# Optimization experiments

Hardware: AMD Instinct MI355X
Metric: run time of the kernel (lower is better)

The kernel has to match this reference:

```python
import jax, jax.numpy as jnp
import numpy as np

K = 3  # number of propagation hops in SGConv


def setup_inputs() -> dict:
    key = jax.random.key(0)
    k1, k2, k3, k4 = jax.random.split(key, 4)
    N, E, F_in, F_out = 100000, 1600000, 32, 64
    x = jax.random.normal(k1, (N, F_in), dtype=jnp.float32)
    edge_index = jax.random.randint(k2, (2, E), 0, N, dtype=jnp.int64)
    # Linear(in_channels, hidden_channels) params, torch layout: W [out, in], b [out]
    lim = 1.0 / np.sqrt(F_in)
    W = jax.random.uniform(k3, (F_out, F_in), minval=-lim, maxval=lim, dtype=jnp.float32)
    b = jax.random.uniform(k4, (F_out,), minval=-lim, maxval=lim, dtype=jnp.float32)
    return {"x": x, "edge_index": edge_index, "W": W, "b": b}


def reference(x, edge_index, W, b):
    N = x.shape[0]
    # gcn_norm: add self-loops with weight 1, symmetric normalization
    loop = jnp.arange(N, dtype=edge_index.dtype)
    src = jnp.concatenate([edge_index[0], loop])  # [E+N] message sources (x_j)
    dst = jnp.concatenate([edge_index[1], loop])  # [E+N] aggregation targets
    ones = jnp.ones(src.shape[0], dtype=x.dtype)
    deg = jax.ops.segment_sum(ones, dst, num_segments=N)  # in-degree incl. self-loop
    dinv = jnp.where(deg > 0, jax.lax.rsqrt(deg), 0.0)
    norm = dinv[src] * dinv[dst]  # [E+N]
    # K hops of normalized sparse propagation: x <- \hat{A} x
    h = x
    for _ in range(K):
        h = jax.ops.segment_sum(norm[:, None] * h[src], dst, num_segments=N)
    # final linear transform
    return h @ W.T + b
```

## Files before the change

### kernel.cpp

```cpp
#include <hip/hip_runtime.h>


#define F_IN 32
#define F_OUT 64
#define SB_SHIFT 13
#define MAXSB 16
#define SUB_SHIFT 9
#define SUB (1 << SUB_SHIFT)
#define EPB1 2048
#define EPB2 4096
#define SCAP 147456
#define SUBCAP 12288
#define BPS (SCAP / EPB2)

typedef float f4 __attribute__((ext_vector_type(4)));
typedef _Float16 h4 __attribute__((ext_vector_type(4)));
typedef int i2 __attribute__((ext_vector_type(2)));

__global__ __launch_bounds__(256) void k_bin1(const int* __restrict__ ei,
                                              int* __restrict__ scur,
                                              unsigned* __restrict__ b1, int E) {
    __shared__ unsigned stage[EPB1];
    __shared__ unsigned char bid[EPB1];
    __shared__ int hist[MAXSB], lscan[MAXSB], lbase[MAXSB], fcur[MAXSB];
    int tid = threadIdx.x;
    int base = blockIdx.x * EPB1;
    int cnt = E - base; if (cnt > EPB1) cnt = EPB1;

    if (tid < MAXSB) hist[tid] = 0;
    __syncthreads();
    for (int k = 0; k < EPB1 / 256; ++k) {
        int i = base + k * 256 + tid;
        if (i < E) atomicAdd(&hist[ei[E + i] >> SB_SHIFT], 1);
    }
    __syncthreads();
    if (tid < 64) {
        int c = (tid < MAXSB) ? hist[tid] : 0;
        int inc = c;
#pragma unroll
        for (int off = 1; off < MAXSB; off <<= 1) {
            int t = __shfl_up(inc, off);
            if (tid >= off) inc += t;
        }
        if (tid < MAXSB) {
            lscan[tid] = inc - c;
            fcur[tid] = inc - c;
            lbase[tid] = c ? atomicAdd(&scur[tid], c) : 0;
        }
    }
    __syncthreads();
    for (int k = 0; k < EPB1 / 256; ++k) {
        int i = base + k * 256 + tid;
        if (i < E) {
            unsigned s = (unsigned)ei[i];
            unsigned d = (unsigned)ei[E + i];
            int b = d >> SB_SHIFT;
            int loc = atomicAdd(&fcur[b], 1);
            stage[loc] = (s << SB_SHIFT) | (d & ((1u << SB_SHIFT) - 1));
            bid[loc] = (unsigned char)b;
        }
    }
    __syncthreads();
    for (int k = 0; k < EPB1 / 256; ++k) {
        int idx = k * 256 + tid;
        if (idx < cnt) {
            int b = bid[idx];
            b1[(size_t)b * SCAP + lbase[b] + (idx - lscan[b])] = stage[idx];
        }
    }
}

__global__ __launch_bounds__(256) void k_bin2(const unsigned* __restrict__ b1,
                                              const int* __restrict__ scur,
                                              int* __restrict__ subcur,
                                              unsigned* __restrict__ b2) {
    int sb = blockIdx.x / BPS;
    int base = (blockIdx.x % BPS) * EPB2;
    int count = scur[sb];
    if (base >= count) return;
    int cnt = count - base; if (cnt > EPB2) cnt = EPB2;
    const unsigned* src = b1 + (size_t)sb * SCAP + base;

    __shared__ unsigned stage[EPB2];
    __shared__ unsigned char bid[EPB2];
    __shared__ int hist[16], lscan[16], lbase[16], fcur[16];
    int tid = threadIdx.x;
    if (tid < 16) hist[tid] = 0;
    __syncthreads();
    for (int k = 0; k < EPB2 / 256; ++k) {
        int i = k * 256 + tid;
        if (i < cnt) atomicAdd(&hist[(src[i] >> SUB_SHIFT) & 15], 1);
    }
    __syncthreads();
    if (tid < 64) {
        int c = (tid < 16) ? hist[tid] : 0;
        int inc = c;
#pragma unroll
        for (int off = 1; off < 16; off <<= 1) {
            int t = __shfl_up(inc, off);
            if (tid >= off) inc += t;
        }
        if (tid < 16) {
            lscan[tid] = inc - c;
            fcur[tid] = inc - c;
            lbase[tid] = c ? atomicAdd(&subcur[sb * 16 + tid], c) : 0;
        }
    }
    __syncthreads();
    for (int k = 0; k < EPB2 / 256; ++k) {
        int i = k * 256 + tid;
        if (i < cnt) {
            unsigned r = src[i];
            int b = (r >> SUB_SHIFT) & 15;
            int loc = atomicAdd(&fcur[b], 1);
            stage[loc] = ((r >> SB_SHIFT) << SUB_SHIFT) | (r & (SUB - 1));
            bid[loc] = (unsigned char)b;
        }
    }
    __syncthreads();
    for (int k = 0; k < EPB2 / 256; ++k) {
        int idx = k * 256 + tid;
        if (idx < cnt) {
            int b = bid[idx];
            b2[(size_t)(sb * 16 + b) * SUBCAP + lbase[b] + (idx - lscan[b])] = stage[idx];
        }
    }
}

__global__ __launch_bounds__(512) void k_fill3(const unsigned* __restrict__ b2,
                                               const int* __restrict__ subcur,
                                               float* __restrict__ dinv,
                                               i2* __restrict__ rp2,
                                               int* __restrict__ col, int N) {
    __shared__ unsigned stage[SUBCAP];
    __shared__ int h[SUB];
    __shared__ int wsum[8];
    int tid = threadIdx.x;
    int g = blockIdx.x;
    int count = subcur[g];
    int sbase = g * SUBCAP;

    h[tid] = 0;
    for (int e = tid; e < count; e += 512) stage[e] = b2[(size_t)sbase + e];
    __syncthreads();
    for (int e = tid; e < count; e += 512) atomicAdd(&h[stage[e] & (SUB - 1)], 1);
    __syncthreads();

    int deg = h[tid];
    int lane = tid & 63, wid = tid >> 6;
    int inc = deg;
#pragma unroll
    for (int off = 1; off < 64; off <<= 1) {
        int t = __shfl_up(inc, off);
        if (lane >= off) inc += t;
    }
    if (lane == 63) wsum[wid] = inc;
    __syncthreads();
    if (wid == 0) {
        int v = (lane < 8) ? wsum[lane] : 0;
#pragma unroll
        for (int off = 1; off < 8; off <<= 1) {
            int t = __shfl_up(v, off);
            if (lane >= off) v += t;
        }
        if (lane < 8) wsum[lane] = v;
    }
    __syncthreads();
    int incl = inc + (wid ? wsum[wid - 1] : 0);
    int excl = incl - deg;

    int node = (g << SUB_SHIFT) + tid;
    if (node < N) {
        dinv[node] = rsqrtf(1.0f + (float)deg);
        rp2[node] = (i2){sbase + excl, sbase + incl};
    }
    h[tid] = excl;
    __syncthreads();

    for (int e = tid; e < count; e += 512) {
        unsigned r = stage[e];
        int slot = sbase + atomicAdd(&h[r & (SUB - 1)], 1);
        col[slot] = (int)(r >> SUB_SHIFT);
    }
}

__global__ void k_prescale(const f4* __restrict__ x, const float* __restrict__ dinv,
                           h4* __restrict__ g, int N8) {
    int t = blockIdx.x * blockDim.x + threadIdx.x;
    if (t < N8) {
        f4 v = dinv[t >> 3] * x[t];
        g[t] = __builtin_convertvector(v, h4);
    }
}

__global__ __launch_bounds__(256) void k_hop_gather(const i2* __restrict__ rp2,
                                                    const int* __restrict__ col,
                                                    const float* __restrict__ dinv,
                                                    const h4* __restrict__ gin,
                                                    h4* __restrict__ gout,
                                                    int N, int final_hop) {
    int t = blockIdx.x * blockDim.x + threadIdx.x;
    int n = t >> 3;
    if (n >= N) return;
    int q = t & 7;
    i2 r2 = rp2[n];
    int e0 = r2.x, e1 = r2.y;
    f4 a0 = __builtin_convertvector(gin[n * 8 + q], f4);
    f4 a1 = {0.f, 0.f, 0.f, 0.f};
    int e = e0;
    for (; e + 3 < e1; e += 4) {
        int s0 = col[e], s1 = col[e + 1], s2 = col[e + 2], s3 = col[e + 3];
        h4 h0 = gin[s0 * 8 + q];
        h4 h1 = gin[s1 * 8 + q];
        h4 h2 = gin[s2 * 8 + q];
        h4 h3 = gin[s3 * 8 + q];
        a0 += __builtin_convertvector(h0, f4);
        a1 += __builtin_convertvector(h1, f4);
        a0 += __builtin_convertvector(h2, f4);
        a1 += __builtin_convertvector(h3, f4);
    }
    for (; e < e1; ++e) a0 += __builtin_convertvector(gin[col[e] * 8 + q], f4);
    float di = dinv[n];
    float sc = final_hop ? di : di * di;
    f4 r = sc * (a0 + a1);
    gout[n * 8 + q] = __builtin_convertvector(r, h4);
}

__global__ __launch_bounds__(256) void k_linear(const _Float16* __restrict__ h,
                                                const float* __restrict__ W,
                                                const float* __restrict__ b,
                                                float* __restrict__ out, int N) {
    __shared__ float Wl[F_OUT][F_IN + 1];
    __shared__ float hl[4][F_IN];
    int tid = threadIdx.x;
    for (int idx = tid; idx < F_OUT * F_IN; idx += 256) {
        Wl[idx >> 5][idx & 31] = W[idx];
    }
    int node0 = blockIdx.x * 4;
    if (tid < 4 * F_IN) {
        int n = tid >> 5, f = tid & 31;
        int node = node0 + n;
        hl[n][f] = (node < N) ? (float)h[node * F_IN + f] : 0.0f;
    }
    __syncthreads();
    int n = tid >> 6;
    int o = tid & 63;
    int node = node0 + n;
    if (node < N) {
        float acc = b[o];
#pragma unroll
        for (int f = 0; f < F_IN; ++f) acc += hl[n][f] * Wl[o][f];
        out[node * F_OUT + o] = acc;
    }
}

extern "C" void kernel_launch(void* const* d_in, const int* in_sizes, int n_in,
                              void* d_out, int out_size, void* d_ws, size_t ws_size,
                              hipStream_t stream) {
    const float* x  = (const float*)d_in[0];
    const int*   ei = (const int*)d_in[1];
    const float* W  = (const float*)d_in[2];
    const float* b  = (const float*)d_in[3];
    float* out = (float*)d_out;

    const int N = in_sizes[0] / F_IN;
    const int E = in_sizes[1] / 2;
    const int NSB  = (N + (1 << SB_SHIFT) - 1) >> SB_SHIFT;
    const int NSUB = (N + SUB - 1) >> SUB_SHIFT;

    int* scur   = (int*)d_ws;
    int* subcur = scur + MAXSB;
    i2*  rp2    = (i2*)(subcur + MAXSB * 16);
    float* dinv = (float*)(rp2 + N);
    unsigned* b1 = (unsigned*)(((uintptr_t)(dinv + N) + 255) & ~(uintptr_t)255);
    unsigned* b2 = b1 + (size_t)MAXSB * SCAP;
    int* col     = (int*)(b2 + (size_t)MAXSB * 16 * SUBCAP);
    _Float16* hA = (_Float16*)(((uintptr_t)(col + (size_t)MAXSB * 16 * SUBCAP) + 255)
                               & ~(uintptr_t)255);
    _Float16* hB  = hA + (size_t)N * F_IN;
    _Float16* hB2 = hB + (size_t)N * F_IN;

    const int B = 256;
    dim3 blk(B);

    hipMemsetAsync(scur, 0, (MAXSB + MAXSB * 16) * sizeof(int), stream);

    k_bin1<<<dim3((E + EPB1 - 1) / EPB1), blk, 0, stream>>>(ei, scur, b1, E);
    k_bin2<<<dim3(NSB * BPS), blk, 0, stream>>>(b1, scur, subcur, b2);

    k_fill3<<<dim3(NSUB), dim3(512), 0, stream>>>(b2, subcur, dinv, rp2, col, N);

    const int N8 = N * 8;
    k_prescale<<<dim3((N8 + B - 1) / B), blk, 0, stream>>>((const f4*)x, dinv, (h4*)hA, N8);

    dim3 gHop(((size_t)N * 8 + B - 1) / B);
    k_hop_gather<<<gHop, blk, 0, stream>>>(rp2, col, dinv, (const h4*)hA, (h4*)hB, N, 0);
    k_hop_gather<<<gHop, blk, 0, stream>>>(rp2, col, dinv, (const h4*)hB, (h4*)hB2, N, 0);
    k_hop_gather<<<gHop, blk, 0, stream>>>(rp2, col, dinv, (const h4*)hB2, (h4*)hA, N, 1);

    k_linear<<<dim3((N + 3) / 4), blk, 0, stream>>>(hA, W, b, out, N);
}
```

Baseline: 223.6 us.

## Fuse final hop with linear layer and cache edge records in registers during binning

The third propagation hop is merged with the final linear transform. Each block gathers 32 nodes into shared memory and computes 8 outputs per thread, which removes the fp16 round trip of the last hop and one kernel launch. The binning kernels now keep the records loaded in the histogram pass in registers instead of reading global memory a second time, and bin2 drops the shared bucket-id array by recomputing the bucket from the staged record. The fused kernel reloads W into shared memory for every 32 nodes and does more register work per thread.

Result: faster. 212.3 us (-5.1%).

```diff
diff --git a/kernel.cpp b/kernel.cpp
--- a/kernel.cpp
+++ b/kernel.cpp
@@ -21,17 +21,28 @@
                                               int* __restrict__ scur,
                                               unsigned* __restrict__ b1, int E) {
     __shared__ unsigned stage[EPB1];
-    __shared__ unsigned char bid[EPB1];
+    __shared__ unsigned char bidl[EPB1];
     __shared__ int hist[MAXSB], lscan[MAXSB], lbase[MAXSB], fcur[MAXSB];
+    unsigned rec[EPB1 / 256];
+    int      bk[EPB1 / 256];
     int tid = threadIdx.x;
     int base = blockIdx.x * EPB1;
     int cnt = E - base; if (cnt > EPB1) cnt = EPB1;
 
     if (tid < MAXSB) hist[tid] = 0;
     __syncthreads();
+#pragma unroll
     for (int k = 0; k < EPB1 / 256; ++k) {
         int i = base + k * 256 + tid;
-        if (i < E) atomicAdd(&hist[ei[E + i] >> SB_SHIFT], 1);
+        bk[k] = -1;
+        if (i < E) {
+            unsigned s = (unsigned)ei[i];
+            unsigned d = (unsigned)ei[E + i];
+            int b = d >> SB_SHIFT;
+            rec[k] = (s << SB_SHIFT) | (d & ((1u << SB_SHIFT) - 1));
+            bk[k] = b;
+            atomicAdd(&hist[b], 1);
+        }
     }
     __syncthreads();
     if (tid < 64) {
@@ -49,22 +60,19 @@
         }
     }
     __syncthreads();
+#pragma unroll
     for (int k = 0; k < EPB1 / 256; ++k) {
-        int i = base + k * 256 + tid;
-        if (i < E) {
-            unsigned s = (unsigned)ei[i];
-            unsigned d = (unsigned)ei[E + i];
-            int b = d >> SB_SHIFT;
-            int loc = atomicAdd(&fcur[b], 1);
-            stage[loc] = (s << SB_SHIFT) | (d & ((1u << SB_SHIFT) - 1));
-            bid[loc] = (unsigned char)b;
+        if (bk[k] >= 0) {
+            int loc = atomicAdd(&fcur[bk[k]], 1);
+            stage[loc] = rec[k];
+            bidl[loc] = (unsigned char)bk[k];
         }
     }
     __syncthreads();
     for (int k = 0; k < EPB1 / 256; ++k) {
         int idx = k * 256 + tid;
         if (idx < cnt) {
-            int b = bid[idx];
+            int b = bidl[idx];
             b1[(size_t)b * SCAP + lbase[b] + (idx - lscan[b])] = stage[idx];
         }
     }
@@ -82,14 +90,20 @@
     const unsigned* src = b1 + (size_t)sb * SCAP + base;
 
     __shared__ unsigned stage[EPB2];
-    __shared__ unsigned char bid[EPB2];
     __shared__ int hist[16], lscan[16], lbase[16], fcur[16];
+    unsigned rec[EPB2 / 256];
     int tid = threadIdx.x;
     if (tid < 16) hist[tid] = 0;
     __syncthreads();
+#pragma unroll
     for (int k = 0; k < EPB2 / 256; ++k) {
         int i = k * 256 + tid;
-        if (i < cnt) atomicAdd(&hist[(src[i] >> SUB_SHIFT) & 15], 1);
+        rec[k] = 0xFFFFFFFFu;
+        if (i < cnt) {
+            unsigned r = src[i];
+            rec[k] = r;
+            atomicAdd(&hist[(r >> SUB_SHIFT) & 15], 1);
+        }
     }
     __syncthreads();
     if (tid < 64) {
@@ -107,22 +121,22 @@
         }
     }
     __syncthreads();
+#pragma unroll
     for (int k = 0; k < EPB2 / 256; ++k) {
-        int i = k * 256 + tid;
-        if (i < cnt) {
-            unsigned r = src[i];
-            int b = (r >> SUB_SHIFT) & 15;
+        if (rec[k] != 0xFFFFFFFFu) {
+            int b = (rec[k] >> SUB_SHIFT) & 15;
             int loc = atomicAdd(&fcur[b], 1);
-            stage[loc] = ((r >> SB_SHIFT) << SUB_SHIFT) | (r & (SUB - 1));
-            bid[loc] = (unsigned char)b;
+            stage[loc] = rec[k];
         }
     }
     __syncthreads();
     for (int k = 0; k < EPB2 / 256; ++k) {
         int idx = k * 256 + tid;
         if (idx < cnt) {
-            int b = bid[idx];
-            b2[(size_t)(sb * 16 + b) * SUBCAP + lbase[b] + (idx - lscan[b])] = stage[idx];
+            unsigned r = stage[idx];
+            int b = (r >> SUB_SHIFT) & 15;
+            unsigned packed = ((r >> SB_SHIFT) << SUB_SHIFT) | (r & (SUB - 1));
+            b2[(size_t)(sb * 16 + b) * SUBCAP + lbase[b] + (idx - lscan[b])] = packed;
         }
     }
 }
@@ -197,8 +211,7 @@
                                                     const int* __restrict__ col,
                                                     const float* __restrict__ dinv,
                                                     const h4* __restrict__ gin,
-                                                    h4* __restrict__ gout,
-                                                    int N, int final_hop) {
+                                                    h4* __restrict__ gout, int N) {
     int t = blockIdx.x * blockDim.x + threadIdx.x;
     int n = t >> 3;
     if (n >= N) return;
@@ -221,36 +234,69 @@
     }
     for (; e < e1; ++e) a0 += __builtin_convertvector(gin[col[e] * 8 + q], f4);
     float di = dinv[n];
-    float sc = final_hop ? di : di * di;
+    float sc = di * di;
     f4 r = sc * (a0 + a1);
     gout[n * 8 + q] = __builtin_convertvector(r, h4);
 }
 
-__global__ __launch_bounds__(256) void k_linear(const _Float16* __restrict__ h,
-                                                const float* __restrict__ W,
-                                                const float* __restrict__ b,
-                                                float* __restrict__ out, int N) {
+__global__ __launch_bounds__(256) void k_hop3_linear(const i2* __restrict__ rp2,
+                                                     const int* __restrict__ col,
+                                                     const float* __restrict__ dinv,
+                                                     const h4* __restrict__ gin,
+                                                     const float* __restrict__ W,
+                                                     const float* __restrict__ bias,
+                                                     float* __restrict__ out, int N) {
     __shared__ float Wl[F_OUT][F_IN + 1];
-    __shared__ float hl[4][F_IN];
+    __shared__ float hl[32][F_IN + 1];
     int tid = threadIdx.x;
-    for (int idx = tid; idx < F_OUT * F_IN; idx += 256) {
+    for (int idx = tid; idx < F_OUT * F_IN; idx += 256)
         Wl[idx >> 5][idx & 31] = W[idx];
-    }
-    int node0 = blockIdx.x * 4;
-    if (tid < 4 * F_IN) {
-        int n = tid >> 5, f = tid & 31;
-        int node = node0 + n;
-        hl[n][f] = (node < N) ? (float)h[node * F_IN + f] : 0.0f;
-    }
-    __syncthreads();
-    int n = tid >> 6;
-    int o = tid & 63;
-    int node = node0 + n;
-    if (node < N) {
-        float acc = b[o];
-#pragma unroll
-        for (int f = 0; f < F_IN; ++f) acc += hl[n][f] * Wl[o][f];
-        out[node * F_OUT + o] = acc;
+
+    int nl = tid >> 3;
+    int q = tid & 7;
+    int n = blockIdx.x * 32 + nl;
+    if (n < N) {
+        i2 r2 = rp2[n];
+        int e0 = r2.x, e1 = r2.y;
+        f4 a0 = __builtin_convertvector(gin[n * 8 + q], f4);
+        f4 a1 = {0.f, 0.f, 0.f, 0.f};
+        int e = e0;
+        for (; e + 3 < e1; e += 4) {
+            int s0 = col[e], s1 = col[e + 1], s2 = col[e + 2], s3 = col[e + 3];
+            h4 h0 = gin[s0 * 8 + q];
+            h4 h1 = gin[s1 * 8 + q];
+            h4 h2 = gin[s2 * 8 + q];
+            h4 h3 = gin[s3 * 8 + q];
+            a0 += __builtin_convertvector(h0, f4);
+            a1 += __builtin_convertvector(h1, f4);
+            a0 += __builtin_convertvector(h2, f4);
+            a1 += __builtin_convertvector(h3, f4);
+        }
+        for (; e < e1; ++e) a0 += __builtin_convertvector(gin[col[e] * 8 + q], f4);
+        float di = dinv[n];
+        f4 r = di * (a0 + a1);
+        hl[nl][q * 4 + 0] = r.x;
+        hl[nl][q * 4 + 1] = r.y;
+        hl[nl][q * 4 + 2] = r.z;
+        hl[nl][q * 4 + 3] = r.w;
+    }
+    __syncthreads();
+    int obase = q * 8;
+    if (n < N) {
+        float acc[8];
+#pragma unroll
+        for (int j = 0; j < 8; ++j) acc[j] = bias[obase + j];
+#pragma unroll
+        for (int f = 0; f < F_IN; ++f) {
+            float hv = hl[nl][f];
+#pragma unroll
+            for (int j = 0; j < 8; ++j) acc[j] += hv * Wl[obase + j][f];
+        }
+        float* op = out + (size_t)n * F_OUT + obase;
+        f4 v0 = {acc[0], acc[1], acc[2], acc[3]};
+        f4 v1 = {acc[4], acc[5], acc[6], acc[7]};
+        *(f4*)op = v0;
+        *(f4*)(op + 4) = v1;
     }
 }
 
@@ -265,7 +311,6 @@
 
     const int N = in_sizes[0] / F_IN;
     const int E = in_sizes[1] / 2;
-    const int NSB  = (N + (1 << SB_SHIFT) - 1) >> SB_SHIFT;
     const int NSUB = (N + SUB - 1) >> SUB_SHIFT;
 
     int* scur   = (int*)d_ws;
@@ -286,7 +331,8 @@
     hipMemsetAsync(scur, 0, (MAXSB + MAXSB * 16) * sizeof(int), stream);
 
     k_bin1<<<dim3((E + EPB1 - 1) / EPB1), blk, 0, stream>>>(ei, scur, b1, E);
-    k_bin2<<<dim3(NSB * BPS), blk, 0, stream>>>(b1, scur, subcur, b2);
+    k_bin2<<<dim3(((N + (1 << SB_SHIFT) - 1) >> SB_SHIFT) * BPS), blk, 0, stream>>>(
+        b1, scur, subcur, b2);
 
     k_fill3<<<dim3(NSUB), dim3(512), 0, stream>>>(b2, subcur, dinv, rp2, col, N);
 
@@ -294,9 +340,9 @@
     k_prescale<<<dim3((N8 + B - 1) / B), blk, 0, stream>>>((const f4*)x, dinv, (h4*)hA, N8);
 
     dim3 gHop(((size_t)N * 8 + B - 1) / B);
-    k_hop_gather<<<gHop, blk, 0, stream>>>(rp2, col, dinv, (const h4*)hA, (h4*)hB, N, 0);
-    k_hop_gather<<<gHop, blk, 0, stream>>>(rp2, col, dinv, (const h4*)hB, (h4*)hB2, N, 0);
-    k_hop_gather<<<gHop, blk, 0, stream>>>(rp2, col, dinv, (const h4*)hB2, (h4*)hA, N, 1);
-
-    k_linear<<<dim3((N + 3) / 4), blk, 0, stream>>>(hA, W, b, out, N);
-}
+    k_hop_gather<<<gHop, blk, 0, stream>>>(rp2, col, dinv, (const h4*)hA, (h4*)hB, N);
+    k_hop_gather<<<gHop, blk, 0, stream>>>(rp2, col, dinv, (const h4*)hB, (h4*)hB2, N);
+
+    k_hop3_linear<<<dim3((N + 31) / 32), blk, 0, stream>>>(rp2, col, dinv,
+                                                           (const h4*)hB2, W, b, out, N);
+}
```
